# Performance work log

Measured on AMD Instinct MI355X. Metric: run time of the kernel, lower is better.

Reference implementation:

```python
import jax, jax.numpy as jnp
import numpy as np

B, S, T, C, Q = 8, 4096, 2048, 256, 256  # batch, ctx_steps, q_steps, context_size, query_size


def setup_inputs() -> dict:
    key = jax.random.key(0)
    k1, k2, k3, k4 = jax.random.split(key, 4)
    context = jax.random.normal(k1, (B, S, C), dtype=jnp.float32)
    query = jax.random.normal(k2, (T, B, Q), dtype=jnp.float32)
    context_mask = jax.random.randint(k3, (B, S), 0, 2).astype(bool)  # True = masked
    W = jax.random.normal(k4, (C, Q), dtype=jnp.float32)  # bilinear weights [context_size, query_size]
    return {"context": context, "query": query, "context_mask": context_mask, "W": W}


def reference(context, query, context_mask, W):
    # temp = 'auto' -> sqrt(query_size)
    temp = jnp.asarray(np.sqrt(Q), dtype=context.dtype)
    # scores[b,t,s] = (context[b,s,:] @ W) . query[t,b,:]
    scores = jnp.einsum('bsc,cq,tbq->bts', context, W, query) / temp
    neg = jnp.finfo(scores.dtype).min
    scores = jnp.where(context_mask[:, None, :], neg, scores)  # mask over ctx_steps
    attn = jax.nn.softmax(scores, axis=2)  # [B, T, S]
    # rows whose entire context is masked -> attention zeroed
    all_masked = jnp.all(context_mask, axis=1)[:, None, None]
    attn = jnp.where(all_masked, jnp.zeros((), attn.dtype), attn)
    composition = jnp.einsum('bts,bsc->btc', attn, context)  # [B, T, C]
    # module returns (attn, composition) permuted to [T, B, ...]
    return attn.transpose(1, 0, 2), composition.transpose(1, 0, 2)
```

## Files before the change

### kernel.cpp

```cpp
#include <hip/hip_runtime.h>

#define B_ 8
#define S_ 4096
#define T_ 2048
#define C_ 256
#define Q_ 256
#define NROW (T_ * B_)

typedef _Float16 f16;
typedef _Float16 f16x8 __attribute__((ext_vector_type(8)));
typedef _Float16 f16x4 __attribute__((ext_vector_type(4)));
typedef _Float16 f16x2 __attribute__((ext_vector_type(2)));
typedef float f32x4 __attribute__((ext_vector_type(4)));

#define MFMA(a, b, c) __builtin_amdgcn_mfma_f32_16x16x32_f16((a), (b), (c), 0, 0, 0)

__global__ void k_mask_mode(const unsigned char* __restrict__ mb, int* __restrict__ mode,
                            int* __restrict__ allm) {
  __shared__ int s0_, s123_;
  if (threadIdx.x == 0) { s0_ = 0; s123_ = 0; }
  __syncthreads();
  int a0 = 0, a123 = 0;
  int base = threadIdx.x * 128;
  for (int i = 0; i < 128; ++i) {
    int idx = base + i;
    int v = mb[idx];
    if (idx & 3) a123 |= v; else a0 |= v;
  }
  if (a0) atomicOr(&s0_, 1);
  if (a123) atomicOr(&s123_, 1);
  __syncthreads();
  if (threadIdx.x == 0) {
    int m;
    if (s123_ == 0 && s0_ == 0) m = 3;
    else if (s123_ == 0) m = 0;
    else if (s0_ == 0) m = 2;
    else m = 1;
    *mode = m;
  }
  if (threadIdx.x < B_) allm[threadIdx.x] = 1;
}

__global__ void k_expand_mask(const void* __restrict__ mp, const int* __restrict__ mode,
                              float* __restrict__ maskf, int* __restrict__ allm) {
  int i = blockIdx.x * 256 + threadIdx.x;
  int md = *mode;
  int m;
  if (md == 0)      m = ((const int*)mp)[i] != 0;
  else if (md == 1) m = ((const unsigned char*)mp)[i] != 0;
  else if (md == 2) m = ((const float*)mp)[i] != 0.0f;
  else              m = 0;
  maskf[i] = m ? 1.0f : 0.0f;
  if (!m) atomicAnd(&allm[i / S_], 0);
}

__global__ void k_conv_w(const float* __restrict__ W, f16* __restrict__ WT) {
  int i = blockIdx.x * 256 + threadIdx.x;
  int c = i >> 8, q = i & 255;
  WT[q * C_ + c] = (f16)W[i];
}

__global__ void k_conv_q(const float* __restrict__ q, f16* __restrict__ qT) {
  int i = blockIdx.x * 256 + threadIdx.x;
  int e = i * 4;
  int t = e / (B_ * Q_);
  int rb = e - t * (B_ * Q_);
  int b = rb >> 8;
  int qq = rb & 255;
  f32x4 v = *(const f32x4*)(q + e);
  f16x4 h; h[0] = (f16)v[0]; h[1] = (f16)v[1]; h[2] = (f16)v[2]; h[3] = (f16)v[3];
  *(f16x4*)(qT + ((size_t)(b * T_ + t)) * Q_ + qq) = h;
}

__global__ void k_transpose_ctx(const float* __restrict__ ctx, f16* __restrict__ ctxT) {
  __shared__ f16 tile[64][65];
  int s0 = blockIdx.x * 64, c0 = blockIdx.y * 64, b = blockIdx.z;
  int r = threadIdx.x >> 2;
  int cs = (threadIdx.x & 3) * 16;
  const float* src = ctx + ((size_t)(b * S_ + s0 + r)) * C_ + c0 + cs;
  f32x4 v0 = ((const f32x4*)src)[0];
  f32x4 v1 = ((const f32x4*)src)[1];
  f32x4 v2 = ((const f32x4*)src)[2];
  f32x4 v3 = ((const f32x4*)src)[3];
#pragma unroll
  for (int j = 0; j < 4; ++j) {
    tile[r][cs + j] = (f16)v0[j];
    tile[r][cs + 4 + j] = (f16)v1[j];
    tile[r][cs + 8 + j] = (f16)v2[j];
    tile[r][cs + 12 + j] = (f16)v3[j];
  }
  __syncthreads();
  int c = threadIdx.x >> 2;
  int ss = (threadIdx.x & 3) * 16;
  f16x8 o0, o1;
#pragma unroll
  for (int j = 0; j < 8; ++j) { o0[j] = tile[ss + j][c]; o1[j] = tile[ss + 8 + j][c]; }
  f16* dst = ctxT + ((size_t)(b * C_ + c0 + c)) * S_ + s0 + ss;
  *(f16x8*)dst = o0;
  *(f16x8*)(dst + 8) = o1;
}

__launch_bounds__(256, 2)
__global__ void k_gemm_cw(const float* __restrict__ ctx, const f16* __restrict__ WT,
                          f16* __restrict__ CW) {
  __shared__ alignas(16) f16 As[128 * 32];
  __shared__ alignas(16) f16 Bs[128 * 32];
  int n0 = blockIdx.x * 128;
  int m0 = blockIdx.y * 128;
  int tid = threadIdx.x;
  int w = tid >> 6, l = tid & 63;
  int wm = (w >> 1) * 64, wn = (w & 1) * 64;
  int lr = l & 15, lk = (l >> 4) * 8;
  f32x4 acc[4][4] = {};
  for (int k0 = 0; k0 < C_; k0 += 32) {
    __syncthreads();
#pragma unroll
    for (int it = 0; it < 2; ++it) {
      int h = (it * 256 + tid) * 8;
      int row = h >> 5, kk = h & 31;
      const float* ap = ctx + (size_t)(m0 + row) * C_ + k0 + kk;
      f32x4 x0 = ((const f32x4*)ap)[0];
      f32x4 x1 = ((const f32x4*)ap)[1];
      f16x8 hv;
#pragma unroll
      for (int j = 0; j < 4; ++j) { hv[j] = (f16)x0[j]; hv[4 + j] = (f16)x1[j]; }
      *(f16x8*)&As[row * 32 + kk] = hv;
    }
#pragma unroll
    for (int it = 0; it < 2; ++it) {
      int h = (it * 256 + tid) * 8;
      int row = h >> 5, kk = h & 31;
      *(f16x8*)&Bs[row * 32 + kk] = *(const f16x8*)&WT[(size_t)(n0 + row) * C_ + k0 + kk];
    }
    __syncthreads();
    f16x8 af[4], bf[4];
#pragma unroll
    for (int m = 0; m < 4; ++m) af[m] = *(const f16x8*)&As[(wm + m * 16 + lr) * 32 + lk];
#pragma unroll
    for (int n = 0; n < 4; ++n) bf[n] = *(const f16x8*)&Bs[(wn + n * 16 + lr) * 32 + lk];
#pragma unroll
    for (int m = 0; m < 4; ++m)
#pragma unroll
      for (int n = 0; n < 4; ++n) acc[m][n] = MFMA(af[m], bf[n], acc[m][n]);
  }
#pragma unroll
  for (int m = 0; m < 4; ++m)
#pragma unroll
    for (int n = 0; n < 4; ++n)
#pragma unroll
      for (int i = 0; i < 4; ++i) {
        int gm = m0 + wm + m * 16 + (l >> 4) * 4 + i;
        int gn = n0 + wn + n * 16 + lr;
        CW[(size_t)gm * Q_ + gn] = (f16)(acc[m][n][i] * 0.0625f);
      }
}

__launch_bounds__(256, 2)
__global__ void k_gemm_scores(const f16* __restrict__ qT, const f16* __restrict__ CW,
                              const float* __restrict__ maskf, float* __restrict__ attn,
                              float* __restrict__ pmax, float* __restrict__ psum) {
  __shared__ alignas(16) f16 As[128 * 32];
  __shared__ alignas(16) f16 Bs[128 * 32];
  int n0 = blockIdx.x * 128;
  int m0 = blockIdx.y * 128;
  int b = blockIdx.z;
  const f16* A = qT + (size_t)b * T_ * Q_;
  const f16* Bm = CW + (size_t)b * S_ * Q_;
  int tid = threadIdx.x;
  int w = tid >> 6, l = tid & 63;
  int wm = (w >> 1) * 64, wn = (w & 1) * 64;
  int lr = l & 15, lk = (l >> 4) * 8;
  f32x4 acc[4][4] = {};
  for (int k0 = 0; k0 < Q_; k0 += 32) {
    __syncthreads();
#pragma unroll
    for (int it = 0; it < 2; ++it) {
      int h = (it * 256 + tid) * 8;
      int row = h >> 5, kk = h & 31;
      *(f16x8*)&As[row * 32 + kk] = *(const f16x8*)&A[(size_t)(m0 + row) * Q_ + k0 + kk];
    }
#pragma unroll
    for (int it = 0; it < 2; ++it) {
      int h = (it * 256 + tid) * 8;
      int row = h >> 5, kk = h & 31;
      *(f16x8*)&Bs[row * 32 + kk] = *(const f16x8*)&Bm[(size_t)(n0 + row) * Q_ + k0 + kk];
    }
    __syncthreads();
    f16x8 af[4], bf[4];
#pragma unroll
    for (int m = 0; m < 4; ++m) af[m] = *(const f16x8*)&As[(wm + m * 16 + lr) * 32 + lk];
#pragma unroll
    for (int n = 0; n < 4; ++n) bf[n] = *(const f16x8*)&Bs[(wn + n * 16 + lr) * 32 + lk];
#pragma unroll
    for (int m = 0; m < 4; ++m)
#pragma unroll
      for (int n = 0; n < 4; ++n) acc[m][n] = MFMA(af[m], bf[n], acc[m][n]);
  }
  float msk[4];
#pragma unroll
  for (int n = 0; n < 4; ++n) msk[n] = maskf[b * S_ + n0 + wn + n * 16 + lr];
#pragma unroll
  for (int m = 0; m < 4; ++m)
#pragma unroll
    for (int n = 0; n < 4; ++n) {
      int gn = n0 + wn + n * 16 + lr;
#pragma unroll
      for (int i = 0; i < 4; ++i) {
        int gt = m0 + wm + m * 16 + (l >> 4) * 4 + i;
        float v = acc[m][n][i];
        if (msk[n] != 0.0f) v = -3.4e38f;
        acc[m][n][i] = v;
        attn[((size_t)gt * B_ + b) * S_ + gn] = v;
      }
    }
  int g = l >> 4;
  int ch = blockIdx.x * 2 + (w & 1);
#pragma unroll
  for (int m = 0; m < 4; ++m)
#pragma unroll
    for (int i = 0; i < 4; ++i) {
      float mx = fmaxf(fmaxf(acc[m][0][i], acc[m][1][i]), fmaxf(acc[m][2][i], acc[m][3][i]));
      mx = fmaxf(mx, __shfl_xor(mx, 1));
      mx = fmaxf(mx, __shfl_xor(mx, 2));
      mx = fmaxf(mx, __shfl_xor(mx, 4));
      mx = fmaxf(mx, __shfl_xor(mx, 8));
      float sm = 0.0f;
#pragma unroll
      for (int n = 0; n < 4; ++n) sm += __expf(acc[m][n][i] - mx);
      sm += __shfl_xor(sm, 1);
      sm += __shfl_xor(sm, 2);
      sm += __shfl_xor(sm, 4);
      sm += __shfl_xor(sm, 8);
      if (lr == 0) {
        int gt = m0 + wm + m * 16 + g * 4 + i;
        int r = gt * B_ + b;
        pmax[ch * NROW + r] = mx;
        psum[ch * NROW + r] = sm;
      }
    }
}

__launch_bounds__(256, 2)
__global__ void k_gemm_stats(const f16* __restrict__ qT, const f16* __restrict__ CW,
                             const float* __restrict__ maskf,
                             float* __restrict__ pmax, float* __restrict__ psum) {
  __shared__ alignas(16) f16 As[128 * 32];
  __shared__ alignas(16) f16 Bs[128 * 32];
  int n0 = blockIdx.x * 128;
  int m0 = blockIdx.y * 128;
  int b = blockIdx.z;
  const f16* A = qT + (size_t)b * T_ * Q_;
  const f16* Bm = CW + (size_t)b * S_ * Q_;
  int tid = threadIdx.x;
  int w = tid >> 6, l = tid & 63;
  int wm = (w >> 1) * 64, wn = (w & 1) * 64;
  int lr = l & 15, lk = (l >> 4) * 8;
  f32x4 acc[4][4] = {};
  for (int k0 = 0; k0 < Q_; k0 += 32) {
    __syncthreads();
#pragma unroll
    for (int it = 0; it < 2; ++it) {
      int h = (it * 256 + tid) * 8;
      int row = h >> 5, kk = h & 31;
      *(f16x8*)&As[row * 32 + kk] = *(const f16x8*)&A[(size_t)(m0 + row) * Q_ + k0 + kk];
    }
#pragma unroll
    for (int it = 0; it < 2; ++it) {
      int h = (it * 256 + tid) * 8;
      int row = h >> 5, kk = h & 31;
      *(f16x8*)&Bs[row * 32 + kk] = *(const f16x8*)&Bm[(size_t)(n0 + row) * Q_ + k0 + kk];
    }
    __syncthreads();
    f16x8 af[4], bf[4];
#pragma unroll
    for (int m = 0; m < 4; ++m) af[m] = *(const f16x8*)&As[(wm + m * 16 + lr) * 32 + lk];
#pragma unroll
    for (int n = 0; n < 4; ++n) bf[n] = *(const f16x8*)&Bs[(wn + n * 16 + lr) * 32 + lk];
#pragma unroll
    for (int m = 0; m < 4; ++m)
#pragma unroll
      for (int n = 0; n < 4; ++n) acc[m][n] = MFMA(af[m], bf[n], acc[m][n]);
  }
  float msk[4];
#pragma unroll
  for (int n = 0; n < 4; ++n) msk[n] = maskf[b * S_ + n0 + wn + n * 16 + lr];
#pragma unroll
  for (int m = 0; m < 4; ++m)
#pragma unroll
    for (int n = 0; n < 4; ++n) {
      if (msk[n] != 0.0f) {
#pragma unroll
        for (int i = 0; i < 4; ++i) acc[m][n][i] = -3.4e38f;
      }
    }
  int g = l >> 4;
  int ch = blockIdx.x * 2 + (w & 1);
#pragma unroll
  for (int m = 0; m < 4; ++m)
#pragma unroll
    for (int i = 0; i < 4; ++i) {
      float mx = fmaxf(fmaxf(acc[m][0][i], acc[m][1][i]), fmaxf(acc[m][2][i], acc[m][3][i]));
      mx = fmaxf(mx, __shfl_xor(mx, 1));
      mx = fmaxf(mx, __shfl_xor(mx, 2));
      mx = fmaxf(mx, __shfl_xor(mx, 4));
      mx = fmaxf(mx, __shfl_xor(mx, 8));
      float sm = 0.0f;
#pragma unroll
      for (int n = 0; n < 4; ++n) sm += __expf(acc[m][n][i] - mx);
      sm += __shfl_xor(sm, 1);
      sm += __shfl_xor(sm, 2);
      sm += __shfl_xor(sm, 4);
      sm += __shfl_xor(sm, 8);
      if (lr == 0) {
        int gt = m0 + wm + m * 16 + g * 4 + i;
        int r = gt * B_ + b;
        pmax[ch * NROW + r] = mx;
        psum[ch * NROW + r] = sm;
      }
    }
}

__global__ void k_finalize(const float* __restrict__ pmax, const float* __restrict__ psum,
                           float* __restrict__ rmax, float* __restrict__ rsum) {
  int r = blockIdx.x * 256 + threadIdx.x;
  float mx = -3.4e38f;
#pragma unroll 8
  for (int c = 0; c < 64; ++c) mx = fmaxf(mx, pmax[c * NROW + r]);
  float s = 0.0f;
#pragma unroll 8
  for (int c = 0; c < 64; ++c) s += psum[c * NROW + r] * __expf(pmax[c * NROW + r] - mx);
  rmax[r] = mx;
  rsum[r] = s;
}

__launch_bounds__(256, 2)
__global__ void k_comp(float* __restrict__ attn, const f16* __restrict__ ctxT,
                       const float* __restrict__ rmax, const float* __restrict__ rsum,
                       const int* __restrict__ allm, float* __restrict__ comp) {
  __shared__ alignas(16) f16 As[2][32 * 64];
  __shared__ alignas(16) f16 Bs[2][256 * 64];
  const int t0 = blockIdx.x * 32;
  const int b = blockIdx.y;
  const int tid = threadIdx.x;
  const int w = tid >> 6, l = tid & 63;
  const int lr = l & 15, hi = l >> 4;
  const int am = allm[b];
  const int ar = tid >> 4;
  const int cg = tid & 15;
  float mx0, mx1, inv0, inv1;
  float* aP0;
  float* aP1;
  {
    int r0 = (t0 + ar) * B_ + b;
    int r1 = (t0 + 16 + ar) * B_ + b;
    mx0 = rmax[r0]; mx1 = rmax[r1];
    inv0 = am ? 0.0f : (1.0f / rsum[r0]);
    inv1 = am ? 0.0f : (1.0f / rsum[r1]);
    aP0 = attn + (size_t)r0 * S_ + cg * 4;
    aP1 = attn + (size_t)r1 * S_ + cg * 4;
  }
  const int aswz = (cg * 8) ^ ((ar & 7) << 4);
  const int bc = tid >> 3;
  const int bs = tid & 7;
  const f16* bP = ctxT + ((size_t)(b * C_ + bc)) * S_ + bs * 8;
  const int bswz = (bs * 16) ^ ((bc & 7) << 4);
  f32x4 acc[2][4] = {};
  f32x4 aC0 = *(const f32x4*)aP0;
  f32x4 aC1 = *(const f32x4*)aP1;
  f16x8 bC[8];
#pragma unroll
  for (int i = 0; i < 8; ++i) bC[i] = *(const f16x8*)(bP + (size_t)i * 32 * S_);
  for (int k = 0; k < S_ / 64; ++k) {
    const int cur = k & 1;
    const int kn = (k + 1) * 64;
    f32x4 aN0 = *(const f32x4*)(aP0 + kn);
    f32x4 aN1 = *(const f32x4*)(aP1 + kn);
    f16x8 bN[8];
#pragma unroll
    for (int i = 0; i < 8; ++i) bN[i] = *(const f16x8*)(bP + (size_t)i * 32 * S_ + kn);
    f32x4 p0, p1;
#pragma unroll
    for (int e = 0; e < 4; ++e) {
      p0[e] = __expf(aC0[e] - mx0) * inv0;
      p1[e] = __expf(aC1[e] - mx1) * inv1;
    }
    *(f32x4*)(aP0 + k * 64) = p0;
    *(f32x4*)(aP1 + k * 64) = p1;
    f16x4 h0, h1;
#pragma unroll
    for (int e = 0; e < 4; ++e) { h0[e] = (f16)p0[e]; h1[e] = (f16)p1[e]; }
    *(f16x4*)((char*)As[cur] + ar * 128 + aswz) = h0;
    *(f16x4*)((char*)As[cur] + (16 + ar) * 128 + aswz) = h1;
#pragma unroll
    for (int i = 0; i < 8; ++i)
      *(f16x8*)((char*)Bs[cur] + (i * 32 + bc) * 128 + bswz) = bC[i];
    asm volatile("s_waitcnt lgkmcnt(0)" ::: "memory");
    __builtin_amdgcn_s_barrier();
    __builtin_amdgcn_sched_barrier(0);
#pragma unroll
    for (int kk = 0; kk < 2; ++kk) {
      const int cb = (kk * 64 + hi * 16) ^ ((lr & 7) << 4);
      f16x8 af[2], bf[4];
#pragma unroll
      for (int m = 0; m < 2; ++m)
        af[m] = *(const f16x8*)((char*)As[cur] + (m * 16 + lr) * 128 + cb);
#pragma unroll
      for (int n = 0; n < 4; ++n)
        bf[n] = *(const f16x8*)((char*)Bs[cur] + (w * 64 + n * 16 + lr) * 128 + cb);
#pragma unroll
      for (int m = 0; m < 2; ++m)
#pragma unroll
        for (int n = 0; n < 4; ++n) acc[m][n] = MFMA(af[m], bf[n], acc[m][n]);
    }
    aC0 = aN0; aC1 = aN1;
#pragma unroll
    for (int i = 0; i < 8; ++i) bC[i] = bN[i];
  }
#pragma unroll
  for (int m = 0; m < 2; ++m)
#pragma unroll
    for (int n = 0; n < 4; ++n)
#pragma unroll
      for (int i = 0; i < 4; ++i) {
        int tl = m * 16 + hi * 4 + i;
        int cc = w * 64 + n * 16 + lr;
        comp[((size_t)(t0 + tl) * B_ + b) * C_ + cc] = acc[m][n][i];
      }
}

__launch_bounds__(256, 2)
__global__ void k_fused(const f16* __restrict__ qT, const f16* __restrict__ CW,
                        const f16* __restrict__ ctxT, const float* __restrict__ maskf,
                        const float* __restrict__ rmax, const float* __restrict__ rsum,
                        const int* __restrict__ allm,
                        float* __restrict__ attn, float* __restrict__ comp) {
  __shared__ alignas(16) f16 Ps[2][32 * 64];
  const int bid = blockIdx.x;
  const int b = bid & 7, t0 = (bid >> 3) * 32;
  const int tid = threadIdx.x;
  const int w = tid >> 6, l = tid & 63;
  const int lr = l & 15, hi = l >> 4;
  const int rswz = (lr & 7) << 4;
  const int srow = w * 16 + lr;
  const int am = allm[b];
  float smax[2][4], sinv[2][4];
#pragma unroll
  for (int m = 0; m < 2; ++m)
#pragma unroll
    for (int i = 0; i < 4; ++i) {
      int r = (t0 + m * 16 + hi * 4 + i) * B_ + b;
      smax[m][i] = rmax[r];
      sinv[m][i] = am ? 0.0f : (1.0f / rsum[r]);
    }
  f16x8 af[2][8];
#pragma unroll
  for (int m = 0; m < 2; ++m)
#pragma unroll
    for (int kq = 0; kq < 8; ++kq)
      af[m][kq] = *(const f16x8*)(qT + ((size_t)(b * T_ + t0 + m * 16 + lr)) * Q_ + kq * 32 + hi * 8);
  const f16* cwL = CW + (size_t)b * S_ * Q_ + (size_t)srow * Q_ + hi * 8;
  const f16* cxL = ctxT + (size_t)(b * C_ + w * 64 + lr) * S_ + hi * 8;
  const float* maskP = maskf + b * S_ + srow;
  f32x4 accC[2][4] = {};
  f16x8 cwF[8];
#pragma unroll
  for (int kq = 0; kq < 8; ++kq) cwF[kq] = *(const f16x8*)(cwL + kq * 32);
  float mk = maskP[0];
  {
    f16x8 cwN[8];
#pragma unroll
    for (int kq = 0; kq < 8; ++kq) cwN[kq] = *(const f16x8*)(cwL + (size_t)64 * Q_ + kq * 32);
    float mkn = maskP[64];
    f32x4 accS[2] = {};
#pragma unroll
    for (int kq = 0; kq < 8; ++kq)
#pragma unroll
      for (int m = 0; m < 2; ++m) accS[m] = MFMA(af[m][kq], cwF[kq], accS[m]);
#pragma unroll
    for (int m = 0; m < 2; ++m)
#pragma unroll
      for (int i = 0; i < 4; ++i) {
        int tl = m * 16 + hi * 4 + i;
        float p = (mk != 0.0f) ? 0.0f : __expf(accS[m][i] - smax[m][i]) * sinv[m][i];
        float po = __shfl_xor(p, 1);
        if (!(lr & 1)) {
          float2 fp; fp.x = p; fp.y = po;
          *(float2*)&attn[((size_t)(t0 + tl) * B_ + b) * S_ + srow] = fp;
          f16x2 h; h[0] = (f16)p; h[1] = (f16)po;
          *(f16x2*)((char*)Ps[0] + ((tl * 128 + srow * 2) ^ ((tl & 7) << 4))) = h;
        }
      }
#pragma unroll
    for (int kq = 0; kq < 8; ++kq) cwF[kq] = cwN[kq];
    mk = mkn;
    asm volatile("s_waitcnt lgkmcnt(0)" ::: "memory");
    __builtin_amdgcn_s_barrier();
  }
  for (int k = 1; k < S_ / 64; ++k) {
    const int s0 = k * 64;
    const int cur = k & 1, prev = cur ^ 1;
    f16x8 cwN[8];
    float mkn = 0.0f;
    if (k < S_ / 64 - 1) {
#pragma unroll
      for (int kq = 0; kq < 8; ++kq)
        cwN[kq] = *(const f16x8*)(cwL + (size_t)(s0 + 64) * Q_ + kq * 32);
      mkn = maskP[s0 + 64];
    }
    const int sc0 = s0 - 64;
    f16x8 cx[8];
#pragma unroll
    for (int n = 0; n < 4; ++n)
#pragma unroll
      for (int kk = 0; kk < 2; ++kk)
        cx[n * 2 + kk] = *(const f16x8*)(cxL + (size_t)(n * 16) * S_ + sc0 + kk * 32);
    f32x4 accS[2] = {};
#pragma unroll
    for (int kq = 0; kq < 8; ++kq)
#pragma unroll
      for (int m = 0; m < 2; ++m) accS[m] = MFMA(af[m][kq], cwF[kq], accS[m]);
#pragma unroll
    for (int kk = 0; kk < 2; ++kk) {
      f16x8 pa[2];
#pragma unroll
      for (int m = 0; m < 2; ++m)
        pa[m] = *(const f16x8*)((char*)Ps[prev] + (((m * 16 + lr) * 128 + kk * 64 + hi * 16) ^ rswz));
#pragma unroll
      for (int n = 0; n < 4; ++n)
#pragma unroll
        for (int m = 0; m < 2; ++m) accC[m][n] = MFMA(pa[m], cx[n * 2 + kk], accC[m][n]);
    }
#pragma unroll
    for (int m = 0; m < 2; ++m)
#pragma unroll
      for (int i = 0; i < 4; ++i) {
        int tl = m * 16 + hi * 4 + i;
        float p = (mk != 0.0f) ? 0.0f : __expf(accS[m][i] - smax[m][i]) * sinv[m][i];
        float po = __shfl_xor(p, 1);
        if (!(lr & 1)) {
          float2 fp; fp.x = p; fp.y = po;
          *(float2*)&attn[((size_t)(t0 + tl) * B_ + b) * S_ + s0 + srow] = fp;
          f16x2 h; h[0] = (f16)p; h[1] = (f16)po;
          *(f16x2*)((char*)Ps[cur] + ((tl * 128 + srow * 2) ^ ((tl & 7) << 4))) = h;
        }
      }
#pragma unroll
    for (int kq = 0; kq < 8; ++kq) cwF[kq] = cwN[kq];
    mk = mkn;
    asm volatile("s_waitcnt lgkmcnt(0)" ::: "memory");
    __builtin_amdgcn_s_barrier();
  }
  {
    const int sc0 = S_ - 64;
    const int prev = (S_ / 64 - 1) & 1;
    f16x8 cx[8];
#pragma unroll
    for (int n = 0; n < 4; ++n)
#pragma unroll
      for (int kk = 0; kk < 2; ++kk)
        cx[n * 2 + kk] = *(const f16x8*)(cxL + (size_t)(n * 16) * S_ + sc0 + kk * 32);
#pragma unroll
    for (int kk = 0; kk < 2; ++kk) {
      f16x8 pa[2];
#pragma unroll
      for (int m = 0; m < 2; ++m)
        pa[m] = *(const f16x8*)((char*)Ps[prev] + (((m * 16 + lr) * 128 + kk * 64 + hi * 16) ^ rswz));
#pragma unroll
      for (int n = 0; n < 4; ++n)
#pragma unroll
        for (int m = 0; m < 2; ++m) accC[m][n] = MFMA(pa[m], cx[n * 2 + kk], accC[m][n]);
    }
  }
#pragma unroll
  for (int m = 0; m < 2; ++m)
#pragma unroll
    for (int n = 0; n < 4; ++n)
#pragma unroll
      for (int i = 0; i < 4; ++i) {
        int tl = m * 16 + hi * 4 + i;
        int cc = w * 64 + n * 16 + lr;
        comp[((size_t)(t0 + tl) * B_ + b) * C_ + cc] = accC[m][n][i];
      }
}

extern "C" void kernel_launch(void* const* d_in, const int* in_sizes, int n_in,
                              void* d_out, int out_size, void* d_ws, size_t ws_size,
                              hipStream_t stream) {
  const float* ctx = (const float*)d_in[0];
  const float* query = (const float*)d_in[1];
  const void* mask = d_in[2];
  const float* W = (const float*)d_in[3];

  float* out = (float*)d_out;
  float* attn = out;
  float* comp = out + (size_t)T_ * B_ * S_;

  char* ws = (char*)d_ws;
  f16* ctxT = (f16*)(ws);
  f16* qT = (f16*)(ws + 16777216);
  f16* WT = (f16*)(ws + 25165824);
  float* maskf = (float*)(ws + 25296896);
  float* rmax = (float*)(ws + 25427968);
  float* rsum = (float*)(ws + 25493504);
  int* allm = (int*)(ws + 25559040);
  int* mode = (int*)(ws + 25559072);
  float* pmax = (float*)(ws + 25559168);
  float* psum = (float*)(ws + 29753472);

  k_mask_mode<<<1, 256, 0, stream>>>((const unsigned char*)mask, mode, allm);
  k_expand_mask<<<(B_ * S_) / 256, 256, 0, stream>>>(mask, mode, maskf, allm);
  k_conv_w<<<(C_ * Q_) / 256, 256, 0, stream>>>(W, WT);
  k_conv_q<<<(T_ * B_ * Q_ / 4) / 256, 256, 0, stream>>>(query, qT);
  k_transpose_ctx<<<dim3(S_ / 64, C_ / 64, B_), 256, 0, stream>>>(ctx, ctxT);

  if (ws_size >= (size_t)50724992) {
    f16* CW2 = (f16*)(ws + 33947776);
    k_gemm_cw<<<dim3(Q_ / 128, (B_ * S_) / 128), 256, 0, stream>>>(ctx, WT, CW2);
    k_gemm_stats<<<dim3(S_ / 128, T_ / 128, B_), 256, 0, stream>>>(qT, CW2, maskf, pmax, psum);
    k_finalize<<<NROW / 256, 256, 0, stream>>>(pmax, psum, rmax, rsum);
    k_fused<<<dim3((T_ / 32) * B_), 256, 0, stream>>>(qT, CW2, ctxT, maskf, rmax, rsum, allm,
                                                      attn, comp);
  } else {
    f16* CW = (f16*)comp;
    k_gemm_cw<<<dim3(Q_ / 128, (B_ * S_) / 128), 256, 0, stream>>>(ctx, WT, CW);
    k_gemm_scores<<<dim3(S_ / 128, T_ / 128, B_), 256, 0, stream>>>(qT, CW, maskf, attn, pmax, psum);
    k_finalize<<<NROW / 256, 256, 0, stream>>>(pmax, psum, rmax, rsum);
    k_comp<<<dim3(T_ / 32, B_), 256, 0, stream>>>(attn, ctxT, rmax, rsum, allm, comp);
  }
}
```

Measured before the change: 564.0 us.

## Split fused attention kernel over context halves with partial-sum reduction

```diff
diff --git a/kernel.cpp b/kernel.cpp
--- a/kernel.cpp
+++ b/kernel.cpp
@@ -428,15 +428,21 @@
       }
 }
 
-__launch_bounds__(256, 2)
+template <int SP>
+__launch_bounds__(256, 4)
 __global__ void k_fused(const f16* __restrict__ qT, const f16* __restrict__ CW,
                         const f16* __restrict__ ctxT, const float* __restrict__ maskf,
                         const float* __restrict__ rmax, const float* __restrict__ rsum,
                         const int* __restrict__ allm,
-                        float* __restrict__ attn, float* __restrict__ comp) {
+                        float* __restrict__ attn, float* __restrict__ cptr) {
   __shared__ alignas(16) f16 Ps[2][32 * 64];
+  const int CH = S_ / 64 / SP;
   const int bid = blockIdx.x;
-  const int b = bid & 7, t0 = (bid >> 3) * 32;
+  const int b = bid & 7;
+  const int u = bid >> 3;
+  const int t0 = (u % (T_ / 32)) * 32;
+  const int sp = u / (T_ / 32);
+  const int sbase = sp * (S_ / SP);
   const int tid = threadIdx.x;
   const int w = tid >> 6, l = tid & 63;
   const int lr = l & 15, hi = l >> 4;
@@ -458,9 +464,9 @@
 #pragma unroll
     for (int kq = 0; kq < 8; ++kq)
       af[m][kq] = *(const f16x8*)(qT + ((size_t)(b * T_ + t0 + m * 16 + lr)) * Q_ + kq * 32 + hi * 8);
-  const f16* cwL = CW + (size_t)b * S_ * Q_ + (size_t)srow * Q_ + hi * 8;
-  const f16* cxL = ctxT + (size_t)(b * C_ + w * 64 + lr) * S_ + hi * 8;
-  const float* maskP = maskf + b * S_ + srow;
+  const f16* cwL = CW + ((size_t)b * S_ + sbase + srow) * Q_ + hi * 8;
+  const f16* cxL = ctxT + (size_t)(b * C_ + w * 64 + lr) * S_ + sbase + hi * 8;
+  const float* maskP = maskf + b * S_ + sbase + srow;
   f32x4 accC[2][4] = {};
   f16x8 cwF[8];
 #pragma unroll
@@ -471,21 +477,25 @@
 #pragma unroll
     for (int kq = 0; kq < 8; ++kq) cwN[kq] = *(const f16x8*)(cwL + (size_t)64 * Q_ + kq * 32);
     float mkn = maskP[64];
-    f32x4 accS[2] = {};
-#pragma unroll
-    for (int kq = 0; kq < 8; ++kq)
-#pragma unroll
-      for (int m = 0; m < 2; ++m) accS[m] = MFMA(af[m][kq], cwF[kq], accS[m]);
+    f32x4 aS0[2] = {}, aS1[2] = {};
+#pragma unroll
+    for (int kq = 0; kq < 8; kq += 2)
+#pragma unroll
+      for (int m = 0; m < 2; ++m) {
+        aS0[m] = MFMA(af[m][kq], cwF[kq], aS0[m]);
+        aS1[m] = MFMA(af[m][kq + 1], cwF[kq + 1], aS1[m]);
+      }
 #pragma unroll
     for (int m = 0; m < 2; ++m)
 #pragma unroll
       for (int i = 0; i < 4; ++i) {
         int tl = m * 16 + hi * 4 + i;
-        float p = (mk != 0.0f) ? 0.0f : __expf(accS[m][i] - smax[m][i]) * sinv[m][i];
+        float p = (mk != 0.0f) ? 0.0f
+                               : __expf(aS0[m][i] + aS1[m][i] - smax[m][i]) * sinv[m][i];
         float po = __shfl_xor(p, 1);
         if (!(lr & 1)) {
           float2 fp; fp.x = p; fp.y = po;
-          *(float2*)&attn[((size_t)(t0 + tl) * B_ + b) * S_ + srow] = fp;
+          *(float2*)&attn[((size_t)(t0 + tl) * B_ + b) * S_ + sbase + srow] = fp;
           f16x2 h; h[0] = (f16)p; h[1] = (f16)po;
           *(f16x2*)((char*)Ps[0] + ((tl * 128 + srow * 2) ^ ((tl & 7) << 4))) = h;
         }
@@ -496,29 +506,33 @@
     asm volatile("s_waitcnt lgkmcnt(0)" ::: "memory");
     __builtin_amdgcn_s_barrier();
   }
-  for (int k = 1; k < S_ / 64; ++k) {
+#pragma unroll 2
+  for (int k = 1; k < CH; ++k) {
     const int s0 = k * 64;
     const int cur = k & 1, prev = cur ^ 1;
+    const int sc0 = s0 - 64;
+    f16x8 cx[8];
+#pragma unroll
+    for (int n = 0; n < 4; ++n)
+#pragma unroll
+      for (int kk = 0; kk < 2; ++kk)
+        cx[n * 2 + kk] = *(const f16x8*)(cxL + (size_t)(n * 16) * S_ + sc0 + kk * 32);
     f16x8 cwN[8];
     float mkn = 0.0f;
-    if (k < S_ / 64 - 1) {
+    if (k < CH - 1) {
 #pragma unroll
       for (int kq = 0; kq < 8; ++kq)
         cwN[kq] = *(const f16x8*)(cwL + (size_t)(s0 + 64) * Q_ + kq * 32);
       mkn = maskP[s0 + 64];
     }
-    const int sc0 = s0 - 64;
-    f16x8 cx[8];
-#pragma unroll
-    for (int n = 0; n < 4; ++n)
-#pragma unroll
-      for (int kk = 0; kk < 2; ++kk)
-        cx[n * 2 + kk] = *(const f16x8*)(cxL + (size_t)(n * 16) * S_ + sc0 + kk * 32);
-    f32x4 accS[2] = {};
-#pragma unroll
-    for (int kq = 0; kq < 8; ++kq)
-#pragma unroll
-      for (int m = 0; m < 2; ++m) accS[m] = MFMA(af[m][kq], cwF[kq], accS[m]);
+    f32x4 aS0[2] = {}, aS1[2] = {};
+#pragma unroll
+    for (int kq = 0; kq < 8; kq += 2)
+#pragma unroll
+      for (int m = 0; m < 2; ++m) {
+        aS0[m] = MFMA(af[m][kq], cwF[kq], aS0[m]);
+        aS1[m] = MFMA(af[m][kq + 1], cwF[kq + 1], aS1[m]);
+      }
 #pragma unroll
     for (int kk = 0; kk < 2; ++kk) {
       f16x8 pa[2];
@@ -535,11 +549,12 @@
 #pragma unroll
       for (int i = 0; i < 4; ++i) {
         int tl = m * 16 + hi * 4 + i;
-        float p = (mk != 0.0f) ? 0.0f : __expf(accS[m][i] - smax[m][i]) * sinv[m][i];
+        float p = (mk != 0.0f) ? 0.0f
+                               : __expf(aS0[m][i] + aS1[m][i] - smax[m][i]) * sinv[m][i];
         float po = __shfl_xor(p, 1);
         if (!(lr & 1)) {
           float2 fp; fp.x = p; fp.y = po;
-          *(float2*)&attn[((size_t)(t0 + tl) * B_ + b) * S_ + s0 + srow] = fp;
+          *(float2*)&attn[((size_t)(t0 + tl) * B_ + b) * S_ + sbase + s0 + srow] = fp;
           f16x2 h; h[0] = (f16)p; h[1] = (f16)po;
           *(f16x2*)((char*)Ps[cur] + ((tl * 128 + srow * 2) ^ ((tl & 7) << 4))) = h;
         }
@@ -551,8 +566,8 @@
     __builtin_amdgcn_s_barrier();
   }
   {
-    const int sc0 = S_ - 64;
-    const int prev = (S_ / 64 - 1) & 1;
+    const int sc0 = (CH - 1) * 64;
+    const int prev = (CH - 1) & 1;
     f16x8 cx[8];
 #pragma unroll
     for (int n = 0; n < 4; ++n)
@@ -571,6 +586,7 @@
         for (int m = 0; m < 2; ++m) accC[m][n] = MFMA(pa[m], cx[n * 2 + kk], accC[m][n]);
     }
   }
+  float* cout = cptr + (size_t)sp * T_ * B_ * C_;
 #pragma unroll
   for (int m = 0; m < 2; ++m)
 #pragma unroll
@@ -579,8 +595,18 @@
       for (int i = 0; i < 4; ++i) {
         int tl = m * 16 + hi * 4 + i;
         int cc = w * 64 + n * 16 + lr;
-        comp[((size_t)(t0 + tl) * B_ + b) * C_ + cc] = accC[m][n][i];
-      }
+        cout[((size_t)(t0 + tl) * B_ + b) * C_ + cc] = accC[m][n][i];
+      }
+}
+
+__global__ void k_comp_red(const float* __restrict__ P, float* __restrict__ comp) {
+  size_t i = ((size_t)blockIdx.x * 256 + threadIdx.x) * 4;
+  f32x4 a = *(const f32x4*)(P + i);
+  f32x4 c = *(const f32x4*)(P + (size_t)T_ * B_ * C_ + i);
+  f32x4 r;
+#pragma unroll
+  for (int e = 0; e < 4; ++e) r[e] = a[e] + c[e];
+  *(f32x4*)(comp + i) = r;
 }
 
 extern "C" void kernel_launch(void* const* d_in, const int* in_sizes, int n_in,
@@ -613,13 +639,22 @@
   k_conv_q<<<(T_ * B_ * Q_ / 4) / 256, 256, 0, stream>>>(query, qT);
   k_transpose_ctx<<<dim3(S_ / 64, C_ / 64, B_), 256, 0, stream>>>(ctx, ctxT);
 
-  if (ws_size >= (size_t)50724992) {
+  if (ws_size >= (size_t)84279424) {
+    f16* CW2 = (f16*)(ws + 33947776);
+    float* compP = (float*)(ws + 50724992);
+    k_gemm_cw<<<dim3(Q_ / 128, (B_ * S_) / 128), 256, 0, stream>>>(ctx, WT, CW2);
+    k_gemm_stats<<<dim3(S_ / 128, T_ / 128, B_), 256, 0, stream>>>(qT, CW2, maskf, pmax, psum);
+    k_finalize<<<NROW / 256, 256, 0, stream>>>(pmax, psum, rmax, rsum);
+    k_fused<2><<<dim3((T_ / 32) * B_ * 2), 256, 0, stream>>>(qT, CW2, ctxT, maskf, rmax, rsum,
+                                                             allm, attn, compP);
+    k_comp_red<<<(T_ * B_ * C_ / 4) / 256, 256, 0, stream>>>(compP, comp);
+  } else if (ws_size >= (size_t)50724992) {
     f16* CW2 = (f16*)(ws + 33947776);
     k_gemm_cw<<<dim3(Q_ / 128, (B_ * S_) / 128), 256, 0, stream>>>(ctx, WT, CW2);
     k_gemm_stats<<<dim3(S_ / 128, T_ / 128, B_), 256, 0, stream>>>(qT, CW2, maskf, pmax, psum);
     k_finalize<<<NROW / 256, 256, 0, stream>>>(pmax, psum, rmax, rsum);
-    k_fused<<<dim3((T_ / 32) * B_), 256, 0, stream>>>(qT, CW2, ctxT, maskf, rmax, rsum, allm,
-                                                      attn, comp);
+    k_fused<1><<<dim3((T_ / 32) * B_), 256, 0, stream>>>(qT, CW2, ctxT, maskf, rmax, rsum,
+                                                         allm, attn, comp);
   } else {
     f16* CW = (f16*)comp;
     k_gemm_cw<<<dim3(Q_ / 128, (B_ * S_) / 128), 256, 0, stream>>>(ctx, WT, CW);
```

New measurement: 977.3 us. 1.73x slower.
